# Optimization experiments

Hardware: AMD Instinct MI355X
Metric: run time of the kernel (lower is better)

## Reference

```python
import jax, jax.numpy as jnp
import numpy as np

N_NODES, FEAT, EMB, BATCH, NUM_SAMPLE = 100000, 256, 256, 10000, 32


def setup_inputs() -> dict:
    key = jax.random.key(0)
    ks = jax.random.split(key, 8)
    sc = 1.0 / np.sqrt(FEAT).astype(np.float32)
    return {
        "nodes": jax.random.randint(ks[0], (BATCH,), 0, N_NODES),
        "neigh_idx": jax.random.randint(ks[1], (BATCH, NUM_SAMPLE), 0, N_NODES),
        "id2feat": jax.random.normal(ks[2], (N_NODES, FEAT), jnp.float32),
        "Wq": jax.random.normal(ks[3], (FEAT, EMB), jnp.float32) * sc,
        "bq": jnp.zeros((EMB,), jnp.float32),
        "Wk": jax.random.normal(ks[4], (FEAT, EMB), jnp.float32) * sc,
        "bk": jnp.zeros((EMB,), jnp.float32),
        "Wv": jax.random.normal(ks[5], (FEAT, EMB), jnp.float32) * sc,
        "bv": jnp.zeros((EMB,), jnp.float32),
    }


def reference(nodes, neigh_idx, id2feat, Wq, bq, Wk, bk, Wv, bv):
    # Gather: self feats [B, F] and sampled neighbor feats [B, S, F]
    self_feats = id2feat[nodes]
    neigh_feats = id2feat[neigh_idx]
    S = neigh_idx.shape[1]
    # Keys/values over [neighbors, self] -> [B, S+1, F]
    cat = jnp.concatenate([neigh_feats, self_feats[:, None, :]], axis=1)
    Q = self_feats @ Wq + bq               # [B, E]
    K = cat @ Wk + bk                       # [B, S+1, E]
    V = cat @ Wv + bv                       # [B, S+1, E]
    scores = jnp.einsum('be,bse->bs', Q, K)  # [B, S+1]
    # Faithful to original mask loop: with full neighbor lists, columns >= num_sample
    # (the appended self key) are masked out.
    mask = jnp.arange(S + 1) >= S
    scores = jnp.where(mask[None, :], -jnp.inf, scores)
    attn = jax.nn.softmax(scores, axis=-1)   # [B, S+1]
    return jnp.einsum('bs,bse->be', attn, V)  # [B, E]
```

## Files before the change

### kernel.cpp

```cpp
#include <hip/hip_runtime.h>
#include <math.h>

#define F 256
#define E 256
#define S 32
#define CH 4
#define TLP 260

typedef __attribute__((ext_vector_type(8))) short short8;
typedef __attribute__((ext_vector_type(4))) float f32x4;

__device__ __forceinline__ ushort f2bf(float x) {
    uint u = __float_as_uint(x);
    return (ushort)((u + 0x7fffu + ((u >> 16) & 1u)) >> 16);
}
__device__ __forceinline__ float bf2f(ushort h) {
    return __uint_as_float(((uint)h) << 16);
}
__device__ __forceinline__ uint4 pack8(const ushort* h) {
    uint4 r;
    r.x = (uint)h[0] | ((uint)h[1] << 16); r.y = (uint)h[2] | ((uint)h[3] << 16);
    r.z = (uint)h[4] | ((uint)h[5] << 16); r.w = (uint)h[6] | ((uint)h[7] << 16);
    return r;
}
__device__ __forceinline__ void split8(const float* x, short8& h, short8& l) {
    ushort hh[8], ll[8];
#pragma unroll
    for (int i = 0; i < 8; ++i) { hh[i] = f2bf(x[i]); ll[i] = f2bf(x[i] - bf2f(hh[i])); }
    uint4 ph = pack8(hh), pl = pack8(ll);
    h = *reinterpret_cast<short8*>(&ph);
    l = *reinterpret_cast<short8*>(&pl);
}
__device__ __forceinline__ short8 mk8(uint a, uint b, uint c, uint d) {
    uint4 p = make_uint4(a, b, c, d);
    return *reinterpret_cast<short8*>(&p);
}
__device__ __forceinline__ uint pkbf(float v) {
    const ushort h = f2bf(v);
    const ushort l = f2bf(v - bf2f(h));
    return (uint)h | ((uint)l << 16);
}

__global__ __launch_bounds__(512) void prep(const float* __restrict__ Wq,
                                            const float* __restrict__ bq,
                                            const float* __restrict__ Wk,
                                            const float* __restrict__ Wv,
                                            ushort* __restrict__ MTh,
                                            ushort* __restrict__ MTl,
                                            ushort* __restrict__ WvTh,
                                            ushort* __restrict__ WvTl,
                                            float* __restrict__ c) {
    const int blk = blockIdx.x, tid = threadIdx.x;
    const int lane = tid & 63, wave = tid >> 6;
    if (blk < 4) {
        const int wm = wave >> 2, wn = wave & 3;
        const int fr = lane & 15, fk = lane >> 4;
        const int j0 = blk * 64;
        f32x4 acc[2][4];
#pragma unroll
        for (int m = 0; m < 2; ++m)
#pragma unroll
            for (int n = 0; n < 4; ++n) acc[m][n] = (f32x4){0.f, 0.f, 0.f, 0.f};
        for (int k0 = 0; k0 < F; k0 += 32) {
            short8 ah[2], al[2];
#pragma unroll
            for (int m = 0; m < 2; ++m) {
                const float* p = &Wk[(size_t)(j0 + wm * 32 + m * 16 + fr) * F + k0 + fk * 8];
                float x[8];
                *reinterpret_cast<float4*>(&x[0]) = *reinterpret_cast<const float4*>(p);
                *reinterpret_cast<float4*>(&x[4]) = *reinterpret_cast<const float4*>(p + 4);
                split8(x, ah[m], al[m]);
            }
#pragma unroll
            for (int n = 0; n < 4; ++n) {
                const float* p = &Wq[(size_t)(wn * 64 + n * 16 + fr) * F + k0 + fk * 8];
                float x[8];
                *reinterpret_cast<float4*>(&x[0]) = *reinterpret_cast<const float4*>(p);
                *reinterpret_cast<float4*>(&x[4]) = *reinterpret_cast<const float4*>(p + 4);
                short8 bh, bl;
                split8(x, bh, bl);
#pragma unroll
                for (int m = 0; m < 2; ++m) {
                    acc[m][n] = __builtin_amdgcn_mfma_f32_16x16x32_bf16(ah[m], bh, acc[m][n], 0, 0, 0);
                    acc[m][n] = __builtin_amdgcn_mfma_f32_16x16x32_bf16(ah[m], bl, acc[m][n], 0, 0, 0);
                    acc[m][n] = __builtin_amdgcn_mfma_f32_16x16x32_bf16(al[m], bh, acc[m][n], 0, 0, 0);
                }
            }
        }
#pragma unroll
        for (int n = 0; n < 4; ++n) {
            const int i = wn * 64 + n * 16 + fr;
#pragma unroll
            for (int m = 0; m < 2; ++m)
#pragma unroll
                for (int r = 0; r < 4; ++r) {
                    const int j = j0 + wm * 32 + m * 16 + fk * 4 + r;
                    const float v = acc[m][n][r];
                    const ushort h = f2bf(v);
                    MTh[(size_t)j * F + i] = h;
                    MTl[(size_t)j * F + i] = f2bf(v - bf2f(h));
                }
        }
    } else if (blk < 20) {
        __shared__ float t[64][65];
        const int tb = blk - 4;
        const int jt = (tb & 3) * 64, kt = (tb >> 2) * 64;
        const int lk = tid >> 3, lj = (tid & 7) * 8;
        {
            const float* p = &Wv[(size_t)(kt + lk) * E + jt + lj];
            const float4 v0 = *reinterpret_cast<const float4*>(p);
            const float4 v1 = *reinterpret_cast<const float4*>(p + 4);
            t[lk][lj + 0] = v0.x; t[lk][lj + 1] = v0.y; t[lk][lj + 2] = v0.z; t[lk][lj + 3] = v0.w;
            t[lk][lj + 4] = v1.x; t[lk][lj + 5] = v1.y; t[lk][lj + 6] = v1.z; t[lk][lj + 7] = v1.w;
        }
        __syncthreads();
        const int oj = tid >> 3, ok = (tid & 7) * 8;
        ushort h[8], l[8];
#pragma unroll
        for (int u = 0; u < 8; ++u) {
            const float v = t[ok + u][oj];
            h[u] = f2bf(v); l[u] = f2bf(v - bf2f(h[u]));
        }
        *reinterpret_cast<uint4*>(&WvTh[(size_t)(jt + oj) * F + kt + ok]) = pack8(h);
        *reinterpret_cast<uint4*>(&WvTl[(size_t)(jt + oj) * F + kt + ok]) = pack8(l);
    } else {
        __shared__ float bqs[F];
        if (tid < F) bqs[tid] = bq[tid];
        __syncthreads();
        const float4 b4 = *reinterpret_cast<const float4*>(&bqs[lane * 4]);
#pragma unroll
        for (int i = 0; i < 8; ++i) {
            const int j = (blk - 20) * 64 + wave * 8 + i;
            const float4 k4 = *reinterpret_cast<const float4*>(&Wk[(size_t)j * F + lane * 4]);
            float p = k4.x * b4.x + k4.y * b4.y + k4.z * b4.z + k4.w * b4.w;
#pragma unroll
            for (int off = 32; off; off >>= 1) p += __shfl_xor(p, off);
            if (lane == 0) c[j] = p;
        }
    }
}

__device__ __forceinline__ void ld_chunk(float4* d, int idxv, int s0,
                                         const float* __restrict__ t, int lane) {
#pragma unroll
    for (int j = 0; j < CH; ++j) {
        const int nid = __builtin_amdgcn_readlane(idxv, s0 + j);
        d[j] = *reinterpret_cast<const float4*>(&t[(size_t)nid * F + lane * 4]);
    }
}
__device__ __forceinline__ void proc_chunk(const float4* v, const float4 qv,
                                           float& m, float& l, float4& acc) {
#pragma unroll
    for (int j = 0; j < CH; ++j) {
        float p = v[j].x * qv.x + v[j].y * qv.y + v[j].z * qv.z + v[j].w * qv.w;
#pragma unroll
        for (int off = 32; off; off >>= 1) p += __shfl_xor(p, off);
        if (p <= m) {
            const float w = __expf(p - m);
            l += w;
            acc.x += w * v[j].x; acc.y += w * v[j].y;
            acc.z += w * v[j].z; acc.w += w * v[j].w;
        } else {
            const float cc = __expf(m - p);
            l = l * cc + 1.f;
            acc.x = acc.x * cc + v[j].x; acc.y = acc.y * cc + v[j].y;
            acc.z = acc.z * cc + v[j].z; acc.w = acc.w * cc + v[j].w;
            m = p;
        }
    }
}

__global__ __launch_bounds__(512, 4) void fused(const int* __restrict__ nodes,
                                                const int* __restrict__ neigh,
                                                const float* __restrict__ id2feat,
                                                const ushort* __restrict__ MTh,
                                                const ushort* __restrict__ MTl,
                                                const ushort* __restrict__ WvTh,
                                                const ushort* __restrict__ WvTl,
                                                const float* __restrict__ cb,
                                                const float* __restrict__ bv,
                                                float* __restrict__ out,
                                                int B) {
    __shared__ uint tile[64][TLP];

    const int tid = threadIdx.x;
    const int lane = tid & 63, wave = tid >> 6;
    const int wm = wave >> 2, wn = wave & 3;
    const int fr = lane & 15, fk = lane >> 4;
    const int row0 = blockIdx.x * 64;

    int arow[2];
#pragma unroll
    for (int m = 0; m < 2; ++m) {
        const int r = row0 + wm * 32 + m * 16 + fr;
        arow[m] = nodes[r < B ? r : B - 1];
    }
    f32x4 acc[2][4];
#pragma unroll
    for (int m = 0; m < 2; ++m)
#pragma unroll
        for (int n = 0; n < 4; ++n) acc[m][n] = (f32x4){0.f, 0.f, 0.f, 0.f};

    for (int k0 = 0; k0 < F; k0 += 32) {
        short8 ah[2], al[2];
#pragma unroll
        for (int m = 0; m < 2; ++m) {
            const float* p = id2feat + (size_t)arow[m] * F + k0 + fk * 8;
            float x[8];
            *reinterpret_cast<float4*>(&x[0]) = *reinterpret_cast<const float4*>(p);
            *reinterpret_cast<float4*>(&x[4]) = *reinterpret_cast<const float4*>(p + 4);
            split8(x, ah[m], al[m]);
        }
#pragma unroll
        for (int n = 0; n < 4; ++n) {
            const size_t boff = (size_t)(wn * 64 + n * 16 + fr) * F + k0 + fk * 8;
            const short8 bh = *reinterpret_cast<const short8*>(&MTh[boff]);
            const short8 bl = *reinterpret_cast<const short8*>(&MTl[boff]);
#pragma unroll
            for (int m = 0; m < 2; ++m) {
                acc[m][n] = __builtin_amdgcn_mfma_f32_16x16x32_bf16(ah[m], bh, acc[m][n], 0, 0, 0);
                acc[m][n] = __builtin_amdgcn_mfma_f32_16x16x32_bf16(ah[m], bl, acc[m][n], 0, 0, 0);
                acc[m][n] = __builtin_amdgcn_mfma_f32_16x16x32_bf16(al[m], bh, acc[m][n], 0, 0, 0);
            }
        }
    }
#pragma unroll
    for (int n = 0; n < 4; ++n) {
        const int col = wn * 64 + n * 16 + fr;
        const float cc = cb[col];
#pragma unroll
        for (int m = 0; m < 2; ++m)
#pragma unroll
            for (int r = 0; r < 4; ++r)
                tile[wm * 32 + m * 16 + fk * 4 + r][col] = __float_as_uint(acc[m][n][r] + cc);
    }
    __syncthreads();

#pragma unroll 1
    for (int i = 0; i < 8; ++i) {
        const int tr = wave * 8 + i;
        const int node = row0 + tr;
        if (node < B) {
            const int idxv = neigh[node * S + (lane & (S - 1))];
            const uint4 q4 = *reinterpret_cast<const uint4*>(&tile[tr][lane * 4]);
            const float4 qv = make_float4(__uint_as_float(q4.x), __uint_as_float(q4.y),
                                          __uint_as_float(q4.z), __uint_as_float(q4.w));
            float m = -INFINITY, l = 0.f;
            float4 a = make_float4(0.f, 0.f, 0.f, 0.f);
            float4 va[CH], vb[CH];
            ld_chunk(va, idxv, 0, id2feat, lane);
            ld_chunk(vb, idxv, 4, id2feat, lane);
            proc_chunk(va, qv, m, l, a);
            ld_chunk(va, idxv, 8, id2feat, lane);
            proc_chunk(vb, qv, m, l, a);
            ld_chunk(vb, idxv, 12, id2feat, lane);
            proc_chunk(va, qv, m, l, a);
            ld_chunk(va, idxv, 16, id2feat, lane);
            proc_chunk(vb, qv, m, l, a);
            ld_chunk(vb, idxv, 20, id2feat, lane);
            proc_chunk(va, qv, m, l, a);
            ld_chunk(va, idxv, 24, id2feat, lane);
            proc_chunk(vb, qv, m, l, a);
            ld_chunk(vb, idxv, 28, id2feat, lane);
            proc_chunk(va, qv, m, l, a);
            proc_chunk(vb, qv, m, l, a);
            const float inv = 1.0f / l;
            const uint4 o = make_uint4(pkbf(a.x * inv), pkbf(a.y * inv),
                                       pkbf(a.z * inv), pkbf(a.w * inv));
            *reinterpret_cast<uint4*>(&tile[tr][lane * 4]) = o;
        }
    }
    __syncthreads();

#pragma unroll
    for (int m = 0; m < 2; ++m)
#pragma unroll
        for (int n = 0; n < 4; ++n) acc[m][n] = (f32x4){0.f, 0.f, 0.f, 0.f};

    for (int k0 = 0; k0 < F; k0 += 32) {
        short8 ah[2], al[2];
#pragma unroll
        for (int m = 0; m < 2; ++m) {
            const int tr = wm * 32 + m * 16 + fr;
            const uint4 u0 = *reinterpret_cast<const uint4*>(&tile[tr][k0 + fk * 8]);
            const uint4 u1 = *reinterpret_cast<const uint4*>(&tile[tr][k0 + fk * 8 + 4]);
            ah[m] = mk8((u0.x & 0xffffu) | (u0.y << 16), (u0.z & 0xffffu) | (u0.w << 16),
                        (u1.x & 0xffffu) | (u1.y << 16), (u1.z & 0xffffu) | (u1.w << 16));
            al[m] = mk8((u0.x >> 16) | (u0.y & 0xffff0000u), (u0.z >> 16) | (u0.w & 0xffff0000u),
                        (u1.x >> 16) | (u1.y & 0xffff0000u), (u1.z >> 16) | (u1.w & 0xffff0000u));
        }
#pragma unroll
        for (int n = 0; n < 4; ++n) {
            const size_t boff = (size_t)(wn * 64 + n * 16 + fr) * F + k0 + fk * 8;
            const short8 bh = *reinterpret_cast<const short8*>(&WvTh[boff]);
            const short8 bl = *reinterpret_cast<const short8*>(&WvTl[boff]);
#pragma unroll
            for (int m = 0; m < 2; ++m) {
                acc[m][n] = __builtin_amdgcn_mfma_f32_16x16x32_bf16(ah[m], bh, acc[m][n], 0, 0, 0);
                acc[m][n] = __builtin_amdgcn_mfma_f32_16x16x32_bf16(ah[m], bl, acc[m][n], 0, 0, 0);
                acc[m][n] = __builtin_amdgcn_mfma_f32_16x16x32_bf16(al[m], bh, acc[m][n], 0, 0, 0);
            }
        }
    }
#pragma unroll
    for (int n = 0; n < 4; ++n) {
        const int col = wn * 64 + n * 16 + fr;
        const float bb = bv[col];
#pragma unroll
        for (int m = 0; m < 2; ++m)
#pragma unroll
            for (int r = 0; r < 4; ++r) {
                const int grow = row0 + wm * 32 + m * 16 + fk * 4 + r;
                if (grow < B) out[(size_t)grow * E + col] = acc[m][n][r] + bb;
            }
    }
}

extern "C" void kernel_launch(void* const* d_in, const int* in_sizes, int n_in,
                              void* d_out, int out_size, void* d_ws, size_t ws_size,
                              hipStream_t stream) {
    const int*   nodes   = (const int*)d_in[0];
    const int*   neigh   = (const int*)d_in[1];
    const float* id2feat = (const float*)d_in[2];
    const float* Wq      = (const float*)d_in[3];
    const float* bq      = (const float*)d_in[4];
    const float* Wk      = (const float*)d_in[5];
    const float* Wv      = (const float*)d_in[7];
    const float* bv      = (const float*)d_in[8];
    float* out = (float*)d_out;
    const int B = in_sizes[0];

    ushort* MTh  = (ushort*)d_ws;
    ushort* MTl  = MTh + 65536;
    ushort* WvTh = MTl + 65536;
    ushort* WvTl = WvTh + 65536;
    float*  cbuf = (float*)(WvTl + 65536);

    prep<<<dim3(24), dim3(512), 0, stream>>>(Wq, bq, Wk, Wv, MTh, MTl, WvTh, WvTl, cbuf);
    fused<<<dim3((B + 63) / 64), dim3(512), 0, stream>>>(nodes, neigh, id2feat,
                                                         MTh, MTl, WvTh, WvTl,
                                                         cbuf, bv, out, B);
}
```

Before: 145.5 us.

## Shrink fused block to 16 rows and 4 waves for more blocks

Cuts the per-block node tile from 64 to 16 rows and the block from 8 waves to 4. Each wave now owns a 64-column slice and does one 16-row MFMA tile in both GEMM phases, and the attention phase handles 4 nodes per wave instead of 8. The goal is more, smaller blocks (625 instead of 157) so the 256 CUs are better filled and the gather latency is spread more evenly. The cost is that each block rereads the full weight matrices for only 16 rows, so weight traffic from L2 goes up fourfold.

Result: faster. 124.7 us (-14.3%).

```diff
diff --git a/kernel.cpp b/kernel.cpp
--- a/kernel.cpp
+++ b/kernel.cpp
@@ -5,6 +5,7 @@
 #define E 256
 #define S 32
 #define CH 4
+#define NB 16
 #define TLP 260
 
 typedef __attribute__((ext_vector_type(8))) short short8;
@@ -170,75 +171,61 @@
     }
 }
 
-__global__ __launch_bounds__(512, 4) void fused(const int* __restrict__ nodes,
-                                                const int* __restrict__ neigh,
-                                                const float* __restrict__ id2feat,
-                                                const ushort* __restrict__ MTh,
-                                                const ushort* __restrict__ MTl,
-                                                const ushort* __restrict__ WvTh,
-                                                const ushort* __restrict__ WvTl,
-                                                const float* __restrict__ cb,
-                                                const float* __restrict__ bv,
-                                                float* __restrict__ out,
-                                                int B) {
-    __shared__ uint tile[64][TLP];
+__global__ __launch_bounds__(256) void fused(const int* __restrict__ nodes,
+                                             const int* __restrict__ neigh,
+                                             const float* __restrict__ id2feat,
+                                             const ushort* __restrict__ MTh,
+                                             const ushort* __restrict__ MTl,
+                                             const ushort* __restrict__ WvTh,
+                                             const ushort* __restrict__ WvTl,
+                                             const float* __restrict__ cb,
+                                             const float* __restrict__ bv,
+                                             float* __restrict__ out,
+                                             int B) {
+    __shared__ uint tile[NB][TLP];
 
     const int tid = threadIdx.x;
     const int lane = tid & 63, wave = tid >> 6;
-    const int wm = wave >> 2, wn = wave & 3;
     const int fr = lane & 15, fk = lane >> 4;
-    const int row0 = blockIdx.x * 64;
-
-    int arow[2];
-#pragma unroll
-    for (int m = 0; m < 2; ++m) {
-        const int r = row0 + wm * 32 + m * 16 + fr;
-        arow[m] = nodes[r < B ? r : B - 1];
-    }
-    f32x4 acc[2][4];
-#pragma unroll
-    for (int m = 0; m < 2; ++m)
-#pragma unroll
-        for (int n = 0; n < 4; ++n) acc[m][n] = (f32x4){0.f, 0.f, 0.f, 0.f};
+    const int row0 = blockIdx.x * NB;
+
+    const int gr = row0 + fr;
+    const int arow = nodes[gr < B ? gr : B - 1];
+
+    f32x4 acc[4];
+#pragma unroll
+    for (int n = 0; n < 4; ++n) acc[n] = (f32x4){0.f, 0.f, 0.f, 0.f};
 
     for (int k0 = 0; k0 < F; k0 += 32) {
-        short8 ah[2], al[2];
-#pragma unroll
-        for (int m = 0; m < 2; ++m) {
-            const float* p = id2feat + (size_t)arow[m] * F + k0 + fk * 8;
-            float x[8];
-            *reinterpret_cast<float4*>(&x[0]) = *reinterpret_cast<const float4*>(p);
-            *reinterpret_cast<float4*>(&x[4]) = *reinterpret_cast<const float4*>(p + 4);
-            split8(x, ah[m], al[m]);
-        }
+        const float* p = id2feat + (size_t)arow * F + k0 + fk * 8;
+        float x[8];
+        *reinterpret_cast<float4*>(&x[0]) = *reinterpret_cast<const float4*>(p);
+        *reinterpret_cast<float4*>(&x[4]) = *reinterpret_cast<const float4*>(p + 4);
+        short8 ah, al;
+        split8(x, ah, al);
 #pragma unroll
         for (int n = 0; n < 4; ++n) {
-            const size_t boff = (size_t)(wn * 64 + n * 16 + fr) * F + k0 + fk * 8;
+            const size_t boff = (size_t)(wave * 64 + n * 16 + fr) * F + k0 + fk * 8;
             const short8 bh = *reinterpret_cast<const short8*>(&MTh[boff]);
             const short8 bl = *reinterpret_cast<const short8*>(&MTl[boff]);
-#pragma unroll
-            for (int m = 0; m < 2; ++m) {
-                acc[m][n] = __builtin_amdgcn_mfma_f32_16x16x32_bf16(ah[m], bh, acc[m][n], 0, 0, 0);
-                acc[m][n] = __builtin_amdgcn_mfma_f32_16x16x32_bf16(ah[m], bl, acc[m][n], 0, 0, 0);
-                acc[m][n] = __builtin_amdgcn_mfma_f32_16x16x32_bf16(al[m], bh, acc[m][n], 0, 0, 0);
-            }
+            acc[n] = __builtin_amdgcn_mfma_f32_16x16x32_bf16(ah, bh, acc[n], 0, 0, 0);
+            acc[n] = __builtin_amdgcn_mfma_f32_16x16x32_bf16(ah, bl, acc[n], 0, 0, 0);
+            acc[n] = __builtin_amdgcn_mfma_f32_16x16x32_bf16(al, bh, acc[n], 0, 0, 0);
         }
     }
 #pragma unroll
     for (int n = 0; n < 4; ++n) {
-        const int col = wn * 64 + n * 16 + fr;
+        const int col = wave * 64 + n * 16 + fr;
         const float cc = cb[col];
 #pragma unroll
-        for (int m = 0; m < 2; ++m)
-#pragma unroll
-            for (int r = 0; r < 4; ++r)
-                tile[wm * 32 + m * 16 + fk * 4 + r][col] = __float_as_uint(acc[m][n][r] + cc);
+        for (int r = 0; r < 4; ++r)
+            tile[fk * 4 + r][col] = __float_as_uint(acc[n][r] + cc);
     }
     __syncthreads();
 
 #pragma unroll 1
-    for (int i = 0; i < 8; ++i) {
-        const int tr = wave * 8 + i;
+    for (int i = 0; i < 4; ++i) {
+        const int tr = wave * 4 + i;
         const int node = row0 + tr;
         if (node < B) {
             const int idxv = neigh[node * S + (lane & (S - 1))];
@@ -273,46 +260,34 @@
     __syncthreads();
 
 #pragma unroll
-    for (int m = 0; m < 2; ++m)
-#pragma unroll
-        for (int n = 0; n < 4; ++n) acc[m][n] = (f32x4){0.f, 0.f, 0.f, 0.f};
+    for (int n = 0; n < 4; ++n) acc[n] = (f32x4){0.f, 0.f, 0.f, 0.f};
 
     for (int k0 = 0; k0 < F; k0 += 32) {
-        short8 ah[2], al[2];
-#pragma unroll
-        for (int m = 0; m < 2; ++m) {
-            const int tr = wm * 32 + m * 16 + fr;
-            const uint4 u0 = *reinterpret_cast<const uint4*>(&tile[tr][k0 + fk * 8]);
-            const uint4 u1 = *reinterpret_cast<const uint4*>(&tile[tr][k0 + fk * 8 + 4]);
-            ah[m] = mk8((u0.x & 0xffffu) | (u0.y << 16), (u0.z & 0xffffu) | (u0.w << 16),
-                        (u1.x & 0xffffu) | (u1.y << 16), (u1.z & 0xffffu) | (u1.w << 16));
-            al[m] = mk8((u0.x >> 16) | (u0.y & 0xffff0000u), (u0.z >> 16) | (u0.w & 0xffff0000u),
-                        (u1.x >> 16) | (u1.y & 0xffff0000u), (u1.z >> 16) | (u1.w & 0xffff0000u));
-        }
+        const uint4 u0 = *reinterpret_cast<const uint4*>(&tile[fr][k0 + fk * 8]);
+        const uint4 u1 = *reinterpret_cast<const uint4*>(&tile[fr][k0 + fk * 8 + 4]);
+        const short8 ah = mk8((u0.x & 0xffffu) | (u0.y << 16), (u0.z & 0xffffu) | (u0.w << 16),
+                              (u1.x & 0xffffu) | (u1.y << 16), (u1.z & 0xffffu) | (u1.w << 16));
+        const short8 al = mk8((u0.x >> 16) | (u0.y & 0xffff0000u), (u0.z >> 16) | (u0.w & 0xffff0000u),
+                              (u1.x >> 16) | (u1.y & 0xffff0000u), (u1.z >> 16) | (u1.w & 0xffff0000u));
 #pragma unroll
         for (int n = 0; n < 4; ++n) {
-            const size_t boff = (size_t)(wn * 64 + n * 16 + fr) * F + k0 + fk * 8;
+            const size_t boff = (size_t)(wave * 64 + n * 16 + fr) * F + k0 + fk * 8;
             const short8 bh = *reinterpret_cast<const short8*>(&WvTh[boff]);
             const short8 bl = *reinterpret_cast<const short8*>(&WvTl[boff]);
-#pragma unroll
-            for (int m = 0; m < 2; ++m) {
-                acc[m][n] = __builtin_amdgcn_mfma_f32_16x16x32_bf16(ah[m], bh, acc[m][n], 0, 0, 0);
-                acc[m][n] = __builtin_amdgcn_mfma_f32_16x16x32_bf16(ah[m], bl, acc[m][n], 0, 0, 0);
-                acc[m][n] = __builtin_amdgcn_mfma_f32_16x16x32_bf16(al[m], bh, acc[m][n], 0, 0, 0);
-            }
+            acc[n] = __builtin_amdgcn_mfma_f32_16x16x32_bf16(ah, bh, acc[n], 0, 0, 0);
+            acc[n] = __builtin_amdgcn_mfma_f32_16x16x32_bf16(ah, bl, acc[n], 0, 0, 0);
+            acc[n] = __builtin_amdgcn_mfma_f32_16x16x32_bf16(al, bh, acc[n], 0, 0, 0);
         }
     }
 #pragma unroll
     for (int n = 0; n < 4; ++n) {
-        const int col = wn * 64 + n * 16 + fr;
+        const int col = wave * 64 + n * 16 + fr;
         const float bb = bv[col];
 #pragma unroll
-        for (int m = 0; m < 2; ++m)
-#pragma unroll
-            for (int r = 0; r < 4; ++r) {
-                const int grow = row0 + wm * 32 + m * 16 + fk * 4 + r;
-                if (grow < B) out[(size_t)grow * E + col] = acc[m][n][r] + bb;
-            }
+        for (int r = 0; r < 4; ++r) {
+            const int grow = row0 + fk * 4 + r;
+            if (grow < B) out[(size_t)grow * E + col] = acc[n][r] + bb;
+        }
     }
 }
 
@@ -337,7 +312,7 @@
     float*  cbuf = (float*)(WvTl + 65536);
 
     prep<<<dim3(24), dim3(512), 0, stream>>>(Wq, bq, Wk, Wv, MTh, MTl, WvTh, WvTl, cbuf);
-    fused<<<dim3((B + 63) / 64), dim3(512), 0, stream>>>(nodes, neigh, id2feat,
-                                                         MTh, MTl, WvTh, WvTl,
-                                                         cbuf, bv, out, B);
-}
+    fused<<<dim3((B + NB - 1) / NB), dim3(256), 0, stream>>>(nodes, neigh, id2feat,
+                                                             MTh, MTl, WvTh, WvTl,
+                                                             cbuf, bv, out, B);
+}
```
